# Kernel tuning notes

Hardware: AMD Instinct MI355X
Metric: run time of the kernel (lower is better)

The kernel has to match this reference:

```python
import jax, jax.numpy as jnp
import numpy as np

B, S, D = 2, 2048, 1024
H, DK, DV = 16, 64, 64


def setup_inputs() -> dict:
    key = jax.random.key(0)
    ks = jax.random.split(key, 9)
    s = 0.02
    return {
        "x": jax.random.normal(ks[0], (B, S, D), dtype=jnp.float32),
        "mask": jnp.zeros((B, S), dtype=bool),  # True = padded position
        "Wq": jax.random.normal(ks[1], (D, H * DK), dtype=jnp.float32) * s,
        "bq": jnp.zeros((H * DK,), dtype=jnp.float32),
        "Wk": jax.random.normal(ks[2], (D, H * DK), dtype=jnp.float32) * s,
        "bk": jnp.zeros((H * DK,), dtype=jnp.float32),
        "Wv": jax.random.normal(ks[3], (D, H * DV), dtype=jnp.float32) * s,
        "bv": jnp.zeros((H * DV,), dtype=jnp.float32),
        "Wo": jax.random.normal(ks[4], (H * DV, D), dtype=jnp.float32) * s,
        "bo": jnp.zeros((D,), dtype=jnp.float32),
    }


def reference(x, mask, Wq, bq, Wk, bk, Wv, bv, Wo, bo):
    Bx, Sx, _ = x.shape
    # projections -> [B, H, S, dk/dv]
    q = (x @ Wq + bq).reshape(Bx, Sx, H, DK).transpose(0, 2, 1, 3)
    k = (x @ Wk + bk).reshape(Bx, Sx, H, DK).transpose(0, 2, 1, 3)
    v = (x @ Wv + bv).reshape(Bx, Sx, H, DV).transpose(0, 2, 1, 3)
    # scaled QK^T: [B, H, Sq, Sk]
    scores = jnp.einsum("bhqd,bhkd->bhqk", q, k) / jnp.sqrt(jnp.float32(DK))
    neg_inf = jnp.float32(-jnp.inf)
    # padding mask: True masks out key positions
    scores = jnp.where(mask[:, None, None, :], neg_inf, scores)
    # causal mask
    causal = jnp.triu(jnp.ones((Sx, Sx), dtype=bool), k=1)
    scores = jnp.where(causal[None, None, :, :], neg_inf, scores)
    attn = jax.nn.softmax(scores, axis=-1)
    out = jnp.einsum("bhqk,bhkd->bhqd", attn, v)  # [B, H, S, dv]
    out = out.transpose(0, 2, 1, 3).reshape(Bx, Sx, H * DV)
    return out @ Wo + bo
```

## Files before the change

kernel.cpp:

```cpp
#include <hip/hip_runtime.h>
#include <stdint.h>

typedef __bf16 bf16_t;
typedef __bf16 bf16x8 __attribute__((ext_vector_type(8)));
typedef float f32x4 __attribute__((ext_vector_type(4)));

#define S_LEN 2048
#define D_MODEL 1024
#define NH 16
#define DKV 64
#define BATCH 2

#define QSCALE 0.1803368801111204f

__device__ __forceinline__ uint16_t f2bfu(float f) {
    union { float f; uint32_t u; } c; c.f = f;
    return (uint16_t)((c.u + 0x7fffu + ((c.u >> 16) & 1u)) >> 16);
}
__device__ __forceinline__ bf16_t f2bf(float f) {
    union { uint16_t s; bf16_t b; } o; o.s = f2bfu(f);
    return o.b;
}
__device__ __forceinline__ uint32_t pack2t(float lo, float hi) {
    union { float f; uint32_t u; } a, b; a.f = lo; b.f = hi;
    return (a.u >> 16) | (b.u & 0xFFFF0000u);
}
__device__ __forceinline__ void gld_lds16(const bf16_t* g, bf16_t* l) {
    __builtin_amdgcn_global_load_lds(
        (const __attribute__((address_space(1))) void*)g,
        (__attribute__((address_space(3))) void*)l, 16, 0, 0);
}

__global__ __launch_bounds__(256) void k_convert_x(const float* __restrict__ x,
                                                   bf16_t* __restrict__ xb, int n) {
    int i = (blockIdx.x * 256 + threadIdx.x) * 4;
    if (i < n) {
        float4 v = *(const float4*)(x + i);
        xb[i + 0] = f2bf(v.x);
        xb[i + 1] = f2bf(v.y);
        xb[i + 2] = f2bf(v.z);
        xb[i + 3] = f2bf(v.w);
    }
}

__global__ __launch_bounds__(256) void k_transpose3(const float* __restrict__ W0,
                                                    const float* __restrict__ W1,
                                                    const float* __restrict__ W2,
                                                    bf16_t* __restrict__ WT) {
    __shared__ float tile[64][65];
    int k0 = blockIdx.x * 64;
    int n0 = blockIdx.y * 64;
    const float* W = (n0 < 1024) ? W0 : (n0 < 2048) ? W1 : W2;
    int np = n0 & 1023;
    int tx = threadIdx.x & 63, ty = threadIdx.x >> 6;
    #pragma unroll
    for (int r = ty; r < 64; r += 4)
        tile[r][tx] = W[(size_t)(k0 + r) * 1024 + np + tx];
    __syncthreads();
    #pragma unroll
    for (int r = ty; r < 64; r += 4)
        WT[(size_t)(n0 + r) * 1024 + k0 + tx] = f2bf(tile[tx][r]);
}

__global__ __launch_bounds__(256) void k_transpose_v(const bf16_t* __restrict__ V,
                                                     bf16_t* __restrict__ Vt) {
    __shared__ bf16_t tile[64][72];
    int st = blockIdx.x, bh = blockIdx.y;
    int t = threadIdx.x;
    int c = (t & 7) * 8;
    const bf16_t* src = V + ((size_t)bh * S_LEN + st * 64) * DKV;
    #pragma unroll
    for (int p = 0; p < 2; p++) {
        int r = p * 32 + (t >> 3);
        *(uint4*)&tile[r][c] = *(const uint4*)&src[(size_t)r * 64 + c];
    }
    __syncthreads();
    #pragma unroll
    for (int p = 0; p < 2; p++) {
        int d = p * 32 + (t >> 3);
        union { uint16_t s[8]; uint4 u; } pk;
        #pragma unroll
        for (int j = 0; j < 8; j++) {
            union { bf16_t b; uint16_t s; } cv; cv.b = tile[c + j][d];
            pk.s[j] = cv.s;
        }
        *(uint4*)&Vt[((size_t)bh * DKV + d) * S_LEN + st * 64 + c] = pk.u;
    }
}

#define BM 128
#define BN 128
#define BKK 64

template <int MODE>
__global__ __launch_bounds__(256) void k_gemm_bt(
    const bf16_t* __restrict__ A, const bf16_t* __restrict__ BT,
    int M, int N, int K,
    const float* __restrict__ bias0, const float* __restrict__ bias1,
    const float* __restrict__ bias2,
    float* __restrict__ outF,
    bf16_t* __restrict__ outQ, bf16_t* __restrict__ outK, bf16_t* __restrict__ outV) {
    __shared__ __align__(16) bf16_t As[BM * BKK];
    __shared__ __align__(16) bf16_t Bs[BN * BKK];
    int m0 = blockIdx.x * BM;
    int n0 = blockIdx.y * BN;
    int t = threadIdx.x;
    int wid = t >> 6, lane = t & 63, l15 = lane & 15, quad = lane >> 4;
    int wr = (wid >> 1) * 64, wc = (wid & 1) * 64;
    int srow = t >> 3;
    int schunk = (t & 7) ^ (srow & 7);
    int sldst = (t & 7) * 8;
    const f32x4 fzero = {0.f, 0.f, 0.f, 0.f};
    f32x4 acc[4][4];
    #pragma unroll
    for (int i = 0; i < 4; i++)
        #pragma unroll
        for (int j = 0; j < 4; j++) acc[i][j] = fzero;

    int r7 = l15 & 7;
    for (int k0 = 0; k0 < K; k0 += BKK) {
        #pragma unroll
        for (int p = 0; p < 4; p++) {
            int r = p * 32 + srow;
            gld_lds16(&A[(size_t)(m0 + r) * K + k0 + schunk * 8], &As[r * 64 + sldst]);
            gld_lds16(&BT[(size_t)(n0 + r) * K + k0 + schunk * 8], &Bs[r * 64 + sldst]);
        }
        __syncthreads();
        #pragma unroll
        for (int kk = 0; kk < BKK; kk += 32) {
            int g = quad + (kk >> 3);
            int col = ((g ^ r7) << 3);
            bf16x8 af[4], bfr[4];
            #pragma unroll
            for (int mt = 0; mt < 4; mt++)
                af[mt] = *(const bf16x8*)&As[(wr + mt * 16 + l15) * 64 + col];
            #pragma unroll
            for (int nt = 0; nt < 4; nt++)
                bfr[nt] = *(const bf16x8*)&Bs[(wc + nt * 16 + l15) * 64 + col];
            #pragma unroll
            for (int mt = 0; mt < 4; mt++)
                #pragma unroll
                for (int nt = 0; nt < 4; nt++)
                    acc[mt][nt] = __builtin_amdgcn_mfma_f32_16x16x32_bf16(
                        af[mt], bfr[nt], acc[mt][nt], 0, 0, 0);
        }
        __syncthreads();
    }

    #pragma unroll
    for (int mt = 0; mt < 4; mt++) {
        #pragma unroll
        for (int nt = 0; nt < 4; nt++) {
            #pragma unroll
            for (int r = 0; r < 4; r++) {
                int gr = m0 + wr + mt * 16 + quad * 4 + r;
                int gc = n0 + wc + nt * 16 + l15;
                float val = acc[mt][nt][r];
                if (MODE == 0) {
                    int sec = gc >> 10;
                    int nn = gc & 1023;
                    const float* bias = (sec == 0) ? bias0 : (sec == 1) ? bias1 : bias2;
                    val += bias[nn];
                    int b = gr >> 11, s = gr & 2047;
                    int h = nn >> 6, d = nn & 63;
                    size_t idx = (((size_t)(b * NH + h)) * S_LEN + s) * DKV + d;
                    if (sec == 0)      outQ[idx] = f2bf(val * QSCALE);
                    else if (sec == 1) outK[idx] = f2bf(val);
                    else               outV[idx] = f2bf(val);
                } else {
                    outF[(size_t)gr * N + gc] = val + bias0[gc];
                }
            }
        }
    }
}

#define APD 72
#define VPD 136

__global__ __launch_bounds__(256) void k_attn5(
    const bf16_t* __restrict__ Q, const bf16_t* __restrict__ Kg,
    const bf16_t* __restrict__ Vt, const unsigned char* __restrict__ mask,
    bf16_t* __restrict__ O) {
    __shared__ __align__(16) char qps_raw[64 * APD * sizeof(bf16_t)];
    bf16_t (*Qs)[APD] = (bf16_t(*)[APD])qps_raw;
    bf16_t (*Ps)[16][APD] = (bf16_t(*)[16][APD])qps_raw;
    __shared__ bf16_t Ks[128][APD];
    __shared__ bf16_t Vs[64][VPD];
    __shared__ float maskS[128];

    int bid = blockIdx.x;
    int bh = bid & 31;
    int qt = 31 - (bid >> 5);
    int b = bh >> 4, h = bh & 15;
    int t = threadIdx.x;
    int w = t >> 6, lane = t & 63, l15 = lane & 15, quad = lane >> 4;

    const bf16_t* Qbase = Q + ((size_t)bh * S_LEN + qt * 64) * DKV;
    {
        int r = t >> 3, c = (t & 7) * 8;
        *(uint4*)&Qs[r][c]      = *(const uint4*)&Qbase[(size_t)r * 64 + c];
        *(uint4*)&Qs[r + 32][c] = *(const uint4*)&Qbase[(size_t)(r + 32) * 64 + c];
    }
    __syncthreads();
    bf16x8 qf0 = *(const bf16x8*)&Qs[w * 16 + l15][quad * 8];
    bf16x8 qf1 = *(const bf16x8*)&Qs[w * 16 + l15][32 + quad * 8];

    const f32x4 fzero = {0.f, 0.f, 0.f, 0.f};
    f32x4 oacc[4];
    f32x4 lacc = fzero;
    #pragma unroll
    for (int nt = 0; nt < 4; nt++) oacc[nt] = fzero;

    const bf16_t one_b = (bf16_t)1.0f;
    const bf16x8 onesf = {one_b, one_b, one_b, one_b, one_b, one_b, one_b, one_b};

    int qg   = qt * 64 + w * 16 + l15;
    int qmin = qt * 64 + w * 16;
    int qmax = qmin + 15;
    int ktmax = qt >> 1;

    for (int kt = 0; kt <= ktmax; kt++) {
        __syncthreads();
        {
            int r = t >> 3, c = (t & 7) * 8;
            const bf16_t* Kb = Kg + ((size_t)bh * S_LEN + kt * 128) * DKV;
            #pragma unroll
            for (int p = 0; p < 4; p++)
                *(uint4*)&Ks[r + p * 32][c] = *(const uint4*)&Kb[(size_t)(r + p * 32) * 64 + c];
            int d = t >> 4, vc = (t & 15) * 8;
            #pragma unroll
            for (int p = 0; p < 4; p++)
                *(uint4*)&Vs[d + p * 16][vc] =
                    *(const uint4*)&Vt[((size_t)bh * DKV + d + p * 16) * S_LEN + kt * 128 + vc];
        }
        if (t < 128) maskS[t] = mask[b * S_LEN + kt * 128 + t] ? -1e30f : 0.0f;
        __syncthreads();

        #pragma unroll
        for (int sub = 0; sub < 2; sub++) {
            int kbase = kt * 128 + sub * 64;
            if (kbase > qmax) break;

            f32x4 sacc[4];
            #pragma unroll
            for (int mt = 0; mt < 4; mt++) sacc[mt] = fzero;
            #pragma unroll
            for (int kk = 0; kk < 64; kk += 32) {
                bf16x8 qf = kk ? qf1 : qf0;
                #pragma unroll
                for (int mt = 0; mt < 4; mt++) {
                    bf16x8 af = *(const bf16x8*)&Ks[sub * 64 + mt * 16 + l15][kk + quad * 8];
                    sacc[mt] = __builtin_amdgcn_mfma_f32_16x16x32_bf16(af, qf, sacc[mt], 0, 0, 0);
                }
            }

            bool diag = (kbase + 63 > qmin);
            #pragma unroll
            for (int mt = 0; mt < 4; mt++) {
                float4 m4 = *(const float4*)&maskS[sub * 64 + mt * 16 + quad * 4];
                #pragma unroll
                for (int r = 0; r < 4; r++)
                    sacc[mt][r] += ((const float*)&m4)[r];
                if (diag) {
                    int kgb = kbase + mt * 16 + quad * 4;
                    #pragma unroll
                    for (int r = 0; r < 4; r++)
                        if (kgb + r > qg) sacc[mt][r] = -1e30f;
                }
            }
            #pragma unroll
            for (int mt = 0; mt < 4; mt++) {
                uint32_t p0 = pack2t(exp2f(sacc[mt][0]), exp2f(sacc[mt][1]));
                uint32_t p1 = pack2t(exp2f(sacc[mt][2]), exp2f(sacc[mt][3]));
                union { uint32_t u[2]; uint2 v; } pk; pk.u[0] = p0; pk.u[1] = p1;
                *(uint2*)&Ps[w][l15][mt * 16 + quad * 4] = pk.v;
            }

            #pragma unroll
            for (int kk = 0; kk < 64; kk += 32) {
                bf16x8 pf = *(const bf16x8*)&Ps[w][l15][kk + quad * 8];
                #pragma unroll
                for (int nt = 0; nt < 4; nt++) {
                    bf16x8 vf = *(const bf16x8*)&Vs[nt * 16 + l15][sub * 64 + kk + quad * 8];
                    oacc[nt] = __builtin_amdgcn_mfma_f32_16x16x32_bf16(pf, vf, oacc[nt], 0, 0, 0);
                }
                lacc = __builtin_amdgcn_mfma_f32_16x16x32_bf16(pf, onesf, lacc, 0, 0, 0);
            }
        }
    }

    #pragma unroll
    for (int r = 0; r < 4; r++) {
        float l = lacc[r];
        float invl = l > 0.f ? 1.f / l : 0.f;
        int q = qt * 64 + w * 16 + quad * 4 + r;
        #pragma unroll
        for (int nt = 0; nt < 4; nt++) {
            int d = nt * 16 + l15;
            O[((size_t)b * S_LEN + q) * D_MODEL + h * DKV + d] = f2bf(oacc[nt][r] * invl);
        }
    }
}

extern "C" void kernel_launch(void* const* d_in, const int* in_sizes, int n_in,
                              void* d_out, int out_size, void* d_ws, size_t ws_size,
                              hipStream_t stream) {
    const float* x = (const float*)d_in[0];
    const unsigned char* mask = (const unsigned char*)d_in[1];
    const float* Wq = (const float*)d_in[2];
    const float* bq = (const float*)d_in[3];
    const float* Wk = (const float*)d_in[4];
    const float* bk = (const float*)d_in[5];
    const float* Wv = (const float*)d_in[6];
    const float* bv = (const float*)d_in[7];
    const float* Wo = (const float*)d_in[8];
    const float* bo = (const float*)d_in[9];
    float* out = (float*)d_out;

    char* ws = (char*)d_ws;
    const size_t MB = 1024 * 1024;
    bf16_t* xb    = (bf16_t*)(ws + 0 * MB);
    bf16_t* Vtb   = (bf16_t*)(ws + 0 * MB);
    bf16_t* WqkvT = (bf16_t*)(ws + 8 * MB);
    bf16_t* WoT   = (bf16_t*)(ws + 14 * MB);
    bf16_t* Qb    = (bf16_t*)(ws + 16 * MB);
    bf16_t* Kb    = (bf16_t*)(ws + 24 * MB);
    bf16_t* Vb    = (bf16_t*)(ws + 32 * MB);
    bf16_t* AOb   = (bf16_t*)(ws + 40 * MB);

    k_convert_x<<<dim3(4096), dim3(256), 0, stream>>>(x, xb, 4 * 1024 * 1024);
    k_transpose3<<<dim3(16, 48), dim3(256), 0, stream>>>(Wq, Wk, Wv, WqkvT);
    k_transpose3<<<dim3(16, 16), dim3(256), 0, stream>>>(Wo, Wo, Wo, WoT);
    k_gemm_bt<0><<<dim3(32, 24), dim3(256), 0, stream>>>(
        xb, WqkvT, 4096, 3072, 1024, bq, bk, bv, nullptr, Qb, Kb, Vb);
    k_transpose_v<<<dim3(32, 32), dim3(256), 0, stream>>>(Vb, Vtb);
    k_attn5<<<dim3(1024), dim3(256), 0, stream>>>(Qb, Kb, Vtb, mask, AOb);
    k_gemm_bt<1><<<dim3(32, 8), dim3(256), 0, stream>>>(
        AOb, WoT, 4096, 1024, 1024, bo, nullptr, nullptr, out,
        nullptr, nullptr, nullptr);
}
```

Measured before the change: 212.9 us.

## Fuse V transpose into QKV GEMM epilogue, restructure attention K/V loading

Merges the two weight-transpose launches into one and removes the separate V transpose kernel by having the QKV GEMM epilogue write V directly in transposed layout with packed 8-byte stores. The attention kernel now processes 64-key tiles instead of 128. K/V are loaded straight into XOR-swizzled LDS with direct global-to-LDS loads instead of padded arrays. Query tiles are interleaved across the grid to balance causal work. This cuts launches and an intermediate pass over V, but uses more loop iterations with a barrier each.

```diff
diff --git a/kernel.cpp b/kernel.cpp
--- a/kernel.cpp
+++ b/kernel.cpp
@@ -43,15 +43,20 @@
     }
 }
 
-__global__ __launch_bounds__(256) void k_transpose3(const float* __restrict__ W0,
-                                                    const float* __restrict__ W1,
-                                                    const float* __restrict__ W2,
-                                                    bf16_t* __restrict__ WT) {
+__global__ __launch_bounds__(256) void k_transpose4(
+    const float* __restrict__ Wq, const float* __restrict__ Wk,
+    const float* __restrict__ Wv, const float* __restrict__ Wo,
+    bf16_t* __restrict__ WqkvT, bf16_t* __restrict__ WoT) {
     __shared__ float tile[64][65];
     int k0 = blockIdx.x * 64;
     int n0 = blockIdx.y * 64;
-    const float* W = (n0 < 1024) ? W0 : (n0 < 2048) ? W1 : W2;
-    int np = n0 & 1023;
+    const float* W; bf16_t* WT; int np, nw;
+    if (n0 < 3072) {
+        W = (n0 < 1024) ? Wq : (n0 < 2048) ? Wk : Wv;
+        np = n0 & 1023; WT = WqkvT; nw = n0;
+    } else {
+        W = Wo; np = n0 - 3072; WT = WoT; nw = n0 - 3072;
+    }
     int tx = threadIdx.x & 63, ty = threadIdx.x >> 6;
     #pragma unroll
     for (int r = ty; r < 64; r += 4)
@@ -59,33 +64,7 @@
     __syncthreads();
     #pragma unroll
     for (int r = ty; r < 64; r += 4)
-        WT[(size_t)(n0 + r) * 1024 + k0 + tx] = f2bf(tile[tx][r]);
-}
-
-__global__ __launch_bounds__(256) void k_transpose_v(const bf16_t* __restrict__ V,
-                                                     bf16_t* __restrict__ Vt) {
-    __shared__ bf16_t tile[64][72];
-    int st = blockIdx.x, bh = blockIdx.y;
-    int t = threadIdx.x;
-    int c = (t & 7) * 8;
-    const bf16_t* src = V + ((size_t)bh * S_LEN + st * 64) * DKV;
-    #pragma unroll
-    for (int p = 0; p < 2; p++) {
-        int r = p * 32 + (t >> 3);
-        *(uint4*)&tile[r][c] = *(const uint4*)&src[(size_t)r * 64 + c];
-    }
-    __syncthreads();
-    #pragma unroll
-    for (int p = 0; p < 2; p++) {
-        int d = p * 32 + (t >> 3);
-        union { uint16_t s[8]; uint4 u; } pk;
-        #pragma unroll
-        for (int j = 0; j < 8; j++) {
-            union { bf16_t b; uint16_t s; } cv; cv.b = tile[c + j][d];
-            pk.s[j] = cv.s;
-        }
-        *(uint4*)&Vt[((size_t)bh * DKV + d) * S_LEN + st * 64 + c] = pk.u;
-    }
+        WT[(size_t)(nw + r) * 1024 + k0 + tx] = f2bf(tile[tx][r]);
 }
 
 #define BM 128
@@ -99,7 +78,7 @@
     const float* __restrict__ bias0, const float* __restrict__ bias1,
     const float* __restrict__ bias2,
     float* __restrict__ outF,
-    bf16_t* __restrict__ outQ, bf16_t* __restrict__ outK, bf16_t* __restrict__ outV) {
+    bf16_t* __restrict__ outQ, bf16_t* __restrict__ outK, bf16_t* __restrict__ outVt) {
     __shared__ __align__(16) bf16_t As[BM * BKK];
     __shared__ __align__(16) bf16_t Bs[BN * BKK];
     int m0 = blockIdx.x * BM;
@@ -151,47 +130,62 @@
     for (int mt = 0; mt < 4; mt++) {
         #pragma unroll
         for (int nt = 0; nt < 4; nt++) {
-            #pragma unroll
-            for (int r = 0; r < 4; r++) {
-                int gr = m0 + wr + mt * 16 + quad * 4 + r;
+            if (MODE == 0) {
                 int gc = n0 + wc + nt * 16 + l15;
-                float val = acc[mt][nt][r];
-                if (MODE == 0) {
-                    int sec = gc >> 10;
-                    int nn = gc & 1023;
-                    const float* bias = (sec == 0) ? bias0 : (sec == 1) ? bias1 : bias2;
-                    val += bias[nn];
-                    int b = gr >> 11, s = gr & 2047;
-                    int h = nn >> 6, d = nn & 63;
-                    size_t idx = (((size_t)(b * NH + h)) * S_LEN + s) * DKV + d;
-                    if (sec == 0)      outQ[idx] = f2bf(val * QSCALE);
-                    else if (sec == 1) outK[idx] = f2bf(val);
-                    else               outV[idx] = f2bf(val);
+                int sec = gc >> 10;
+                int nn = gc & 1023;
+                int h = nn >> 6, d = nn & 63;
+                int gr0 = m0 + wr + mt * 16 + quad * 4;
+                int b = gr0 >> 11, s0 = gr0 & 2047;
+                if (sec == 2) {
+                    float bv = bias2[nn];
+                    uint32_t lo = (uint32_t)f2bfu(acc[mt][nt][0] + bv) |
+                                  ((uint32_t)f2bfu(acc[mt][nt][1] + bv) << 16);
+                    uint32_t hi = (uint32_t)f2bfu(acc[mt][nt][2] + bv) |
+                                  ((uint32_t)f2bfu(acc[mt][nt][3] + bv) << 16);
+                    uint2 pk; pk.x = lo; pk.y = hi;
+                    *(uint2*)&outVt[(((size_t)(b * NH + h)) * DKV + d) * S_LEN + s0] = pk;
                 } else {
-                    outF[(size_t)gr * N + gc] = val + bias0[gc];
+                    const float* bias = (sec == 0) ? bias0 : bias1;
+                    float bv = bias[nn];
+                    #pragma unroll
+                    for (int r = 0; r < 4; r++) {
+                        float val = acc[mt][nt][r] + bv;
+                        size_t idx = (((size_t)(b * NH + h)) * S_LEN + s0 + r) * DKV + d;
+                        if (sec == 0) outQ[idx] = f2bf(val * QSCALE);
+                        else          outK[idx] = f2bf(val);
+                    }
                 }
+            } else {
+                #pragma unroll
+                for (int r = 0; r < 4; r++) {
+                    int gr = m0 + wr + mt * 16 + quad * 4 + r;
+                    int gc = n0 + wc + nt * 16 + l15;
+                    outF[(size_t)gr * N + gc] = acc[mt][nt][r] + bias0[gc];
+                }
             }
         }
     }
 }
 
 #define APD 72
-#define VPD 136
-
-__global__ __launch_bounds__(256) void k_attn5(
+
+__global__ __launch_bounds__(256) void k_attn7(
     const bf16_t* __restrict__ Q, const bf16_t* __restrict__ Kg,
     const bf16_t* __restrict__ Vt, const unsigned char* __restrict__ mask,
     bf16_t* __restrict__ O) {
     __shared__ __align__(16) char qps_raw[64 * APD * sizeof(bf16_t)];
     bf16_t (*Qs)[APD] = (bf16_t(*)[APD])qps_raw;
     bf16_t (*Ps)[16][APD] = (bf16_t(*)[16][APD])qps_raw;
-    __shared__ bf16_t Ks[128][APD];
-    __shared__ bf16_t Vs[64][VPD];
-    __shared__ float maskS[128];
+    __shared__ __align__(16) bf16_t Ks[64 * 64];
+    __shared__ __align__(16) bf16_t Vs[64 * 64];
+    __shared__ float maskS[64];
 
     int bid = blockIdx.x;
     int bh = bid & 31;
-    int qt = 31 - (bid >> 5);
+    int u = bid >> 5;
+    int a = u & 7, g2 = u >> 3;
+    int qt = (g2 == 0) ? 31 - a : (g2 == 1) ? a : (g2 == 2) ? 23 - a : 8 + a;
     int b = bh >> 4, h = bh & 15;
     int t = threadIdx.x;
     int w = t >> 6, lane = t & 63, l15 = lane & 15, quad = lane >> 4;
@@ -217,76 +211,77 @@
 
     int qg   = qt * 64 + w * 16 + l15;
     int qmin = qt * 64 + w * 16;
-    int qmax = qmin + 15;
-    int ktmax = qt >> 1;
-
-    for (int kt = 0; kt <= ktmax; kt++) {
+    int r7 = l15 & 7;
+
+    int sr = t >> 3;
+    int sc = (t & 7) ^ (sr & 7);
+    int sl = (t & 7) * 8;
+
+    for (int kt = 0; kt <= qt; kt++) {
         __syncthreads();
         {
-            int r = t >> 3, c = (t & 7) * 8;
-            const bf16_t* Kb = Kg + ((size_t)bh * S_LEN + kt * 128) * DKV;
-            #pragma unroll
-            for (int p = 0; p < 4; p++)
-                *(uint4*)&Ks[r + p * 32][c] = *(const uint4*)&Kb[(size_t)(r + p * 32) * 64 + c];
-            int d = t >> 4, vc = (t & 15) * 8;
-            #pragma unroll
-            for (int p = 0; p < 4; p++)
-                *(uint4*)&Vs[d + p * 16][vc] =
-                    *(const uint4*)&Vt[((size_t)bh * DKV + d + p * 16) * S_LEN + kt * 128 + vc];
-        }
-        if (t < 128) maskS[t] = mask[b * S_LEN + kt * 128 + t] ? -1e30f : 0.0f;
+            const bf16_t* Kb = Kg + ((size_t)bh * S_LEN + kt * 64) * DKV;
+            #pragma unroll
+            for (int p = 0; p < 2; p++) {
+                int r = p * 32 + sr;
+                gld_lds16(&Kb[(size_t)r * 64 + sc * 8], &Ks[r * 64 + sl]);
+                gld_lds16(&Vt[((size_t)bh * DKV + r) * S_LEN + kt * 64 + sc * 8],
+                          &Vs[r * 64 + sl]);
+            }
+        }
+        if (t < 64) maskS[t] = mask[b * S_LEN + kt * 64 + t] ? -1e30f : 0.0f;
         __syncthreads();
 
-        #pragma unroll
-        for (int sub = 0; sub < 2; sub++) {
-            int kbase = kt * 128 + sub * 64;
-            if (kbase > qmax) break;
-
-            f32x4 sacc[4];
-            #pragma unroll
-            for (int mt = 0; mt < 4; mt++) sacc[mt] = fzero;
-            #pragma unroll
-            for (int kk = 0; kk < 64; kk += 32) {
-                bf16x8 qf = kk ? qf1 : qf0;
-                #pragma unroll
-                for (int mt = 0; mt < 4; mt++) {
-                    bf16x8 af = *(const bf16x8*)&Ks[sub * 64 + mt * 16 + l15][kk + quad * 8];
-                    sacc[mt] = __builtin_amdgcn_mfma_f32_16x16x32_bf16(af, qf, sacc[mt], 0, 0, 0);
-                }
-            }
-
-            bool diag = (kbase + 63 > qmin);
+        int kbase = kt * 64;
+
+        f32x4 sacc[4];
+        #pragma unroll
+        for (int mt = 0; mt < 4; mt++) sacc[mt] = fzero;
+        #pragma unroll
+        for (int kk = 0; kk < 64; kk += 32) {
+            bf16x8 qf = kk ? qf1 : qf0;
+            int g = quad + (kk >> 3);
+            int col = ((g ^ r7) << 3);
             #pragma unroll
             for (int mt = 0; mt < 4; mt++) {
-                float4 m4 = *(const float4*)&maskS[sub * 64 + mt * 16 + quad * 4];
+                bf16x8 af = *(const bf16x8*)&Ks[(mt * 16 + l15) * 64 + col];
+                sacc[mt] = __builtin_amdgcn_mfma_f32_16x16x32_bf16(af, qf, sacc[mt], 0, 0, 0);
+            }
+        }
+
+        bool diag = (kbase + 63 > qmin);
+        #pragma unroll
+        for (int mt = 0; mt < 4; mt++) {
+            float4 m4 = *(const float4*)&maskS[mt * 16 + quad * 4];
+            #pragma unroll
+            for (int r = 0; r < 4; r++)
+                sacc[mt][r] += ((const float*)&m4)[r];
+            if (diag) {
+                int kgb = kbase + mt * 16 + quad * 4;
                 #pragma unroll
                 for (int r = 0; r < 4; r++)
-                    sacc[mt][r] += ((const float*)&m4)[r];
-                if (diag) {
-                    int kgb = kbase + mt * 16 + quad * 4;
-                    #pragma unroll
-                    for (int r = 0; r < 4; r++)
-                        if (kgb + r > qg) sacc[mt][r] = -1e30f;
-                }
-            }
-            #pragma unroll
-            for (int mt = 0; mt < 4; mt++) {
-                uint32_t p0 = pack2t(exp2f(sacc[mt][0]), exp2f(sacc[mt][1]));
-                uint32_t p1 = pack2t(exp2f(sacc[mt][2]), exp2f(sacc[mt][3]));
-                union { uint32_t u[2]; uint2 v; } pk; pk.u[0] = p0; pk.u[1] = p1;
-                *(uint2*)&Ps[w][l15][mt * 16 + quad * 4] = pk.v;
-            }
-
-            #pragma unroll
-            for (int kk = 0; kk < 64; kk += 32) {
-                bf16x8 pf = *(const bf16x8*)&Ps[w][l15][kk + quad * 8];
-                #pragma unroll
-                for (int nt = 0; nt < 4; nt++) {
-                    bf16x8 vf = *(const bf16x8*)&Vs[nt * 16 + l15][sub * 64 + kk + quad * 8];
-                    oacc[nt] = __builtin_amdgcn_mfma_f32_16x16x32_bf16(pf, vf, oacc[nt], 0, 0, 0);
-                }
-                lacc = __builtin_amdgcn_mfma_f32_16x16x32_bf16(pf, onesf, lacc, 0, 0, 0);
-            }
+                    if (kgb + r > qg) sacc[mt][r] = -1e30f;
+            }
+        }
+        #pragma unroll
+        for (int mt = 0; mt < 4; mt++) {
+            uint32_t p0 = pack2t(exp2f(sacc[mt][0]), exp2f(sacc[mt][1]));
+            uint32_t p1 = pack2t(exp2f(sacc[mt][2]), exp2f(sacc[mt][3]));
+            union { uint32_t u[2]; uint2 v; } pk; pk.u[0] = p0; pk.u[1] = p1;
+            *(uint2*)&Ps[w][l15][mt * 16 + quad * 4] = pk.v;
+        }
+
+        #pragma unroll
+        for (int kk = 0; kk < 64; kk += 32) {
+            bf16x8 pf = *(const bf16x8*)&Ps[w][l15][kk + quad * 8];
+            int g = quad + (kk >> 3);
+            int vcol = ((g ^ r7) << 3);
+            #pragma unroll
+            for (int nt = 0; nt < 4; nt++) {
+                bf16x8 vf = *(const bf16x8*)&Vs[(nt * 16 + l15) * 64 + vcol];
+                oacc[nt] = __builtin_amdgcn_mfma_f32_16x16x32_bf16(pf, vf, oacc[nt], 0, 0, 0);
+            }
+            lacc = __builtin_amdgcn_mfma_f32_16x16x32_bf16(pf, onesf, lacc, 0, 0, 0);
         }
     }
 
@@ -321,21 +316,18 @@
     char* ws = (char*)d_ws;
     const size_t MB = 1024 * 1024;
     bf16_t* xb    = (bf16_t*)(ws + 0 * MB);
-    bf16_t* Vtb   = (bf16_t*)(ws + 0 * MB);
     bf16_t* WqkvT = (bf16_t*)(ws + 8 * MB);
     bf16_t* WoT   = (bf16_t*)(ws + 14 * MB);
     bf16_t* Qb    = (bf16_t*)(ws + 16 * MB);
     bf16_t* Kb    = (bf16_t*)(ws + 24 * MB);
-    bf16_t* Vb    = (bf16_t*)(ws + 32 * MB);
+    bf16_t* Vtb   = (bf16_t*)(ws + 32 * MB);
     bf16_t* AOb   = (bf16_t*)(ws + 40 * MB);
 
     k_convert_x<<<dim3(4096), dim3(256), 0, stream>>>(x, xb, 4 * 1024 * 1024);
-    k_transpose3<<<dim3(16, 48), dim3(256), 0, stream>>>(Wq, Wk, Wv, WqkvT);
-    k_transpose3<<<dim3(16, 16), dim3(256), 0, stream>>>(Wo, Wo, Wo, WoT);
+    k_transpose4<<<dim3(16, 64), dim3(256), 0, stream>>>(Wq, Wk, Wv, Wo, WqkvT, WoT);
     k_gemm_bt<0><<<dim3(32, 24), dim3(256), 0, stream>>>(
-        xb, WqkvT, 4096, 3072, 1024, bq, bk, bv, nullptr, Qb, Kb, Vb);
-    k_transpose_v<<<dim3(32, 32), dim3(256), 0, stream>>>(Vb, Vtb);
-    k_attn5<<<dim3(1024), dim3(256), 0, stream>>>(Qb, Kb, Vtb, mask, AOb);
+        xb, WqkvT, 4096, 3072, 1024, bq, bk, bv, nullptr, Qb, Kb, Vtb);
+    k_attn7<<<dim3(1024), dim3(256), 0, stream>>>(Qb, Kb, Vtb, mask, AOb);
     k_gemm_bt<1><<<dim3(32, 8), dim3(256), 0, stream>>>(
         AOb, WoT, 4096, 1024, 1024, bo, nullptr, nullptr, out,
         nullptr, nullptr, nullptr);
```

Result: faster. 201.9 us (-5.2%).
